# Kernel optimization log

Hardware: AMD Instinct MI355X
Metric: run time of the kernel (lower is better)

## Reference

```python
import jax, jax.numpy as jnp
import numpy as np

HIDDEN = 4096
N_HEADS = 32
N_KV_HEADS = 8
HEAD_DIM = HIDDEN // N_HEADS  # 128
ROPE_THETA = 10000.0
B, S = 2, 2048


def apply_rope_neox(x, positions, theta=ROPE_THETA):
    # x: [B, S, H, D], positions: [S]
    d = x.shape[-1]
    inv_freq = 1.0 / (theta ** (jnp.arange(0, d, 2, dtype=jnp.float32) / d))  # [D/2]
    freqs = positions.astype(jnp.float32)[:, None] * inv_freq                # [S, D/2]
    cos = jnp.cos(freqs)[None, :, None, :]                                   # [1,S,1,D/2]
    sin = jnp.sin(freqs)[None, :, None, :]
    x1, x2 = x[..., : d // 2], x[..., d // 2 :]
    return jnp.concatenate([x1 * cos - x2 * sin, x2 * cos + x1 * sin], axis=-1).astype(x.dtype)


def setup_inputs() -> dict:
    key = jax.random.key(0)
    k1, k2, k3 = jax.random.split(key, 3)
    positions = jnp.arange(S, dtype=jnp.int64) if jax.config.jax_enable_x64 else jnp.arange(S, dtype=jnp.int32)
    hidden_states = jax.random.normal(k1, (B, S, HIDDEN), dtype=jnp.float32)
    q_size = N_HEADS * HEAD_DIM
    kv_size = N_KV_HEADS * HEAD_DIM
    w_qkv = jax.random.normal(k2, (HIDDEN, q_size + 2 * kv_size), dtype=jnp.float32) * (HIDDEN ** -0.5)
    w_o = jax.random.normal(k3, (q_size, HIDDEN), dtype=jnp.float32) * (q_size ** -0.5)
    return {"positions": positions, "hidden_states": hidden_states, "w_qkv": w_qkv, "w_o": w_o}


def reference(positions, hidden_states, w_qkv, w_o):
    q_size = N_HEADS * HEAD_DIM
    kv_size = N_KV_HEADS * HEAD_DIM
    scaling = HEAD_DIM ** -0.5

    # Fused QKV projection
    qkv = jnp.einsum('bsh,hm->bsm', hidden_states, w_qkv)
    q = qkv[..., :q_size].reshape(B, S, N_HEADS, HEAD_DIM)
    k = qkv[..., q_size : q_size + kv_size].reshape(B, S, N_KV_HEADS, HEAD_DIM)
    v = qkv[..., q_size + kv_size :].reshape(B, S, N_KV_HEADS, HEAD_DIM)

    # Neox-style RoPE on q, k
    q = apply_rope_neox(q, positions)
    k = apply_rope_neox(k, positions)

    # GQA: repeat kv heads to match query heads
    rep = N_HEADS // N_KV_HEADS
    k = jnp.repeat(k, rep, axis=2)  # [B,S,Hq,D]
    v = jnp.repeat(v, rep, axis=2)

    # Causal attention (prefill path of PagedAttention)
    scores = jnp.einsum('bqhd,bkhd->bhqk', q, k) * scaling  # [B,H,S,S]
    causal = jnp.tril(jnp.ones((S, S), dtype=bool))
    scores = jnp.where(causal[None, None], scores, jnp.finfo(scores.dtype).min)
    probs = jax.nn.softmax(scores, axis=-1)
    attn = jnp.einsum('bhqk,bkhd->bqhd', probs, v).reshape(B, S, q_size)

    # Output projection
    out = jnp.einsum('bsm,mh->bsh', attn, w_o)
    return out
```

## Files before the change

kernel.cpp:

```cpp
#include <hip/hip_runtime.h>

#define S_LEN 2048
#define NB 2
#define NH 32
#define NKV 8
#define HD 128
#define HID 4096
#define NQKV 6144

using bf16x8 = __attribute__((ext_vector_type(8))) __bf16;
using f32x4  = __attribute__((ext_vector_type(4))) float;

__device__ __forceinline__ ushort f2b(float f) {
  uint u = __builtin_bit_cast(uint, f);
  u += 0x7fffu + ((u >> 16) & 1u);
  return (ushort)(u >> 16);
}
__device__ __forceinline__ float b2f(ushort h) {
  uint u = ((uint)h) << 16;
  return __builtin_bit_cast(float, u);
}

__device__ __forceinline__ uint cvt_pk_bf16(float lo, float hi) {
  uint r;
  asm("v_cvt_pk_bf16_f32 %0, %1, %2" : "=v"(r) : "v"(lo), "v"(hi));
  return r;
}

__device__ __forceinline__ void gld16(const void* g, void* l) {
  __builtin_amdgcn_global_load_lds((const __attribute__((address_space(1))) void*)g,
                                   (__attribute__((address_space(3))) void*)l, 16, 0, 0);
}

__device__ __forceinline__ void stc(float* C, size_t i, float v)  { C[i] = v; }
__device__ __forceinline__ void stc(ushort* C, size_t i, float v) { C[i] = f2b(v); }

__global__ void cvt_bf16(const float* __restrict__ src, ushort* __restrict__ dst, int n) {
  int i = (blockIdx.x * 256 + threadIdx.x) * 4;
  if (i < n) {
    float4 v = *(const float4*)(src + i);
    *(ushort4*)(dst + i) = make_ushort4(f2b(v.x), f2b(v.y), f2b(v.z), f2b(v.w));
  }
}

__global__ void trans_f32_bf16(const float* __restrict__ src, ushort* __restrict__ dst,
                               int R, int C) {
  __shared__ float tile[32][33];
  const int c0 = blockIdx.x * 32, r0 = blockIdx.y * 32;
  const int x = threadIdx.x, y = threadIdx.y;
#pragma unroll
  for (int i = 0; i < 32; i += 8)
    tile[y + i][x] = src[(size_t)(r0 + y + i) * C + (c0 + x)];
  __syncthreads();
#pragma unroll
  for (int i = 0; i < 32; i += 8)
    dst[(size_t)(c0 + y + i) * R + (r0 + x)] = f2b(tile[x][y + i]);
}

__device__ __forceinline__ void stage_tile(const ushort* __restrict__ A,
                                           const ushort* __restrict__ Bt,
                                           int lda, int ldb, int m0, int n0, int kt,
                                           ushort* dA, ushort* dB, int wave, int lane) {
#pragma unroll
  for (int h = 0; h < 4; ++h) {
    const int cb = h * 256 + wave * 64;
    const int c = cb + lane;
    const int row = c >> 3;
    const int kc = (c & 7) ^ (row & 7);
    gld16(A  + (size_t)(m0 + row) * lda + kt + kc * 8, dA + cb * 8);
    gld16(Bt + (size_t)(n0 + row) * ldb + kt + kc * 8, dB + cb * 8);
  }
}

template <typename OutT>
__global__ __launch_bounds__(256, 2) void gemm_p2(const ushort* __restrict__ A,
                                                  const ushort* __restrict__ Bt,
                                                  OutT* __restrict__ C,
                                                  int M, int Ncol, int K,
                                                  int lda, int ldb) {
  __shared__ ushort As[2][128 * 64];
  __shared__ ushort Bs[2][128 * 64];
  const int tid = threadIdx.x, wave = tid >> 6, lane = tid & 63;
  const int lr = lane & 15, lg = lane >> 4;
  const int wm = wave >> 1, wn = wave & 1;
  const int m0 = blockIdx.y * 128, n0 = blockIdx.x * 128;

  f32x4 acc[4][4];
#pragma unroll
  for (int i = 0; i < 4; ++i)
#pragma unroll
    for (int j = 0; j < 4; ++j) acc[i][j] = (f32x4){0.f, 0.f, 0.f, 0.f};

  const int NT = K >> 6;

  stage_tile(A, Bt, lda, ldb, m0, n0, 0, As[0], Bs[0], wave, lane);

  for (int it = 0; it < NT; ++it) {
    const int buf = it & 1;
    if (it + 1 < NT) {
      stage_tile(A, Bt, lda, ldb, m0, n0, (it + 1) << 6, As[buf ^ 1], Bs[buf ^ 1],
                 wave, lane);
      asm volatile("s_waitcnt vmcnt(8)" ::: "memory");
    } else {
      asm volatile("s_waitcnt vmcnt(0)" ::: "memory");
    }
    asm volatile("s_barrier" ::: "memory");

#pragma unroll
    for (int kk = 0; kk < 2; ++kk) {
      bf16x8 af[4], bfr[4];
#pragma unroll
      for (int f = 0; f < 4; ++f) {
        const int row = wm * 64 + f * 16 + lr;
        af[f] = *(const bf16x8*)(&As[buf][row * 64 + (((kk * 4 + lg) ^ (lr & 7)) << 3)]);
      }
#pragma unroll
      for (int g = 0; g < 4; ++g) {
        const int row = wn * 64 + g * 16 + lr;
        bfr[g] = *(const bf16x8*)(&Bs[buf][row * 64 + (((kk * 4 + lg) ^ (lr & 7)) << 3)]);
      }
      __builtin_amdgcn_s_setprio(1);
#pragma unroll
      for (int f = 0; f < 4; ++f)
#pragma unroll
        for (int g = 0; g < 4; ++g)
          acc[f][g] = __builtin_amdgcn_mfma_f32_16x16x32_bf16(af[f], bfr[g], acc[f][g], 0, 0, 0);
      __builtin_amdgcn_s_setprio(0);
    }
    asm volatile("s_barrier" ::: "memory");
  }

#pragma unroll
  for (int f = 0; f < 4; ++f)
#pragma unroll
    for (int g = 0; g < 4; ++g)
#pragma unroll
      for (int r = 0; r < 4; ++r) {
        const int row = m0 + wm * 64 + f * 16 + lg * 4 + r;
        const int col = n0 + wn * 64 + g * 16 + lr;
        stc(C, (size_t)row * Ncol + col, acc[f][g][r]);
      }
}

__global__ __launch_bounds__(256) void rope_qk(ushort* __restrict__ qkv) {
  int t = blockIdx.x * 256 + threadIdx.x;
  const int i = t & 63;
  t >>= 6;
  const int head  = t % (NH + NKV);
  const int token = t / (NH + NKV);
  const int s = token & (S_LEN - 1);
  const size_t base = (size_t)token * NQKV + (head < NH ? head * HD : HID + (head - NH) * HD);
  const float x1 = b2f(qkv[base + i]);
  const float x2 = b2f(qkv[base + 64 + i]);
  const float invf = exp2f(-(float)i * 0.2076205059304602f);
  const float fr = (float)s * invf;
  float cs, sn;
  sincosf(fr, &sn, &cs);
  float o1 = x1 * cs - x2 * sn;
  float o2 = x2 * cs + x1 * sn;
  if (head < NH) {
    o1 *= 0.08838834764831845f;
    o2 *= 0.08838834764831845f;
  }
  qkv[base + i]      = f2b(o1);
  qkv[base + 64 + i] = f2b(o2);
}

__global__ void vtrans(const ushort* __restrict__ qkv, ushort* __restrict__ Vt) {
  __shared__ ushort tile[32][33];
  const int dt = blockIdx.x * 32, st = blockIdx.y * 32, bk = blockIdx.z;
  const int b = bk >> 3, kv = bk & 7;
  const int x = threadIdx.x, y = threadIdx.y;
#pragma unroll
  for (int i = 0; i < 32; i += 8)
    tile[y + i][x] =
        qkv[(size_t)(b * S_LEN + st + y + i) * NQKV + 5120 + kv * HD + dt + x];
  __syncthreads();
#pragma unroll
  for (int i = 0; i < 32; i += 8)
    Vt[((size_t)bk * HD + dt + y + i) * S_LEN + st + x] = tile[x][y + i];
}

__global__ __launch_bounds__(256) void attn_fa(ushort* __restrict__ qkv,
                                               const ushort* __restrict__ Vt) {
  const int lin = blockIdx.x + 32 * blockIdx.y + 256 * blockIdx.z;
  const int swz = (lin & 7) * 64 + (lin >> 3);
  const int qp = swz & 31;
  const int g  = swz >> 5;
  const int kvh = g & 7;
  const int b   = g >> 3;

  const int wid  = threadIdx.x >> 6;
  const int lane = threadIdx.x & 63;
  const int lr = lane & 15, lg = lane >> 4;
  const int h  = kvh * 4 + wid;

  const ushort* K = qkv + (size_t)(b * S_LEN) * NQKV + HID + kvh * HD;
  const ushort* V = Vt + (size_t)(b * NKV + kvh) * (HD * S_LEN);

  __shared__ ushort Ks[2][32 * 128];
  __shared__ ushort Vs[2][128 * 32];
  __shared__ ushort P[4][16 * 40];

  for (int seg = 0; seg < 2; ++seg) {
    const int qt = seg ? (63 - qp) : qp;
    const int q0 = qt * 32;
    const ushort* Q = qkv + (size_t)(b * S_LEN + q0) * NQKV + h * HD;

    bf16x8 qf[2][4];
#pragma unroll
    for (int t = 0; t < 2; ++t)
#pragma unroll
      for (int kb = 0; kb < 4; ++kb)
        qf[t][kb] = *(const bf16x8*)(Q + (size_t)(t * 16 + lr) * NQKV + kb * 32 + lg * 8);

    f32x4 o[2][8];
#pragma unroll
    for (int t = 0; t < 2; ++t)
#pragma unroll
      for (int c = 0; c < 8; ++c) o[t][c] = (f32x4){0.f, 0.f, 0.f, 0.f};
    float mi[2]  = {-1e30f, -1e30f};
    float lip[2] = {0.f, 0.f};

    const int NTk = qt + 1;

#pragma unroll
    for (int it = 0; it < 2; ++it) {
      const int cb = it * 256 + wid * 64;
      const int d = cb + lane;
      const int krow = d >> 4, kslot = d & 15;
      gld16(K + (size_t)krow * NQKV + ((kslot ^ (krow & 15)) * 8), &Ks[0][cb * 8]);
      const int vrow = d >> 2, vslot = d & 3;
      gld16(V + (size_t)vrow * S_LEN + ((vslot ^ ((vrow >> 1) & 3)) * 8), &Vs[0][cb * 8]);
    }

    for (int itk = 0; itk < NTk; ++itk) {
      const int k0 = itk << 5;
      const int bufi = itk & 1;
      if (itk + 1 < NTk) {
        const int kn = k0 + 32;
#pragma unroll
        for (int it = 0; it < 2; ++it) {
          const int cb = it * 256 + wid * 64;
          const int d = cb + lane;
          const int krow = d >> 4, kslot = d & 15;
          gld16(K + (size_t)(kn + krow) * NQKV + ((kslot ^ (krow & 15)) * 8),
                &Ks[bufi ^ 1][cb * 8]);
          const int vrow = d >> 2, vslot = d & 3;
          gld16(V + (size_t)vrow * S_LEN + kn + ((vslot ^ ((vrow >> 1) & 3)) * 8),
                &Vs[bufi ^ 1][cb * 8]);
        }
        asm volatile("s_waitcnt vmcnt(4)" ::: "memory");
      } else {
        asm volatile("s_waitcnt vmcnt(0)" ::: "memory");
      }
      asm volatile("s_barrier" ::: "memory");

      bf16x8 kf[2][4];
#pragma unroll
      for (int u = 0; u < 2; ++u)
#pragma unroll
        for (int kb = 0; kb < 4; ++kb)
          kf[u][kb] = *(const bf16x8*)(
              &Ks[bufi][(u * 16 + lr) * 128 + (((kb * 4 + lg) ^ lr) << 3)]);

      f32x4 s[2][2];
#pragma unroll
      for (int t = 0; t < 2; ++t)
#pragma unroll
        for (int u = 0; u < 2; ++u) s[t][u] = (f32x4){0.f, 0.f, 0.f, 0.f};

      __builtin_amdgcn_s_setprio(1);
#pragma unroll
      for (int kb = 0; kb < 4; ++kb) {
        s[0][0] = __builtin_amdgcn_mfma_f32_16x16x32_bf16(kf[0][kb], qf[0][kb], s[0][0], 0, 0, 0);
        s[1][0] = __builtin_amdgcn_mfma_f32_16x16x32_bf16(kf[0][kb], qf[1][kb], s[1][0], 0, 0, 0);
        s[0][1] = __builtin_amdgcn_mfma_f32_16x16x32_bf16(kf[1][kb], qf[0][kb], s[0][1], 0, 0, 0);
        s[1][1] = __builtin_amdgcn_mfma_f32_16x16x32_bf16(kf[1][kb], qf[1][kb], s[1][1], 0, 0, 0);
      }
      __builtin_amdgcn_s_setprio(0);

      if (k0 == q0) {
#pragma unroll
        for (int t = 0; t < 2; ++t)
#pragma unroll
          for (int u = 0; u < 2; ++u)
#pragma unroll
            for (int r = 0; r < 4; ++r)
              if (u * 16 + lg * 4 + r > t * 16 + lr) s[t][u][r] = -1e30f;
      }

      float pm[2];
#pragma unroll
      for (int t = 0; t < 2; ++t) {
        float a = fmaxf(fmaxf(s[t][0][0], s[t][0][1]), fmaxf(s[t][0][2], s[t][0][3]));
        float c = fmaxf(fmaxf(s[t][1][0], s[t][1][1]), fmaxf(s[t][1][2], s[t][1][3]));
        pm[t] = fmaxf(a, c);
      }

      if (__any((pm[0] > mi[0] + 8.f) || (pm[1] > mi[1] + 8.f))) {
#pragma unroll
        for (int t = 0; t < 2; ++t) {
          float m = pm[t];
          m = fmaxf(m, __shfl_xor(m, 16));
          m = fmaxf(m, __shfl_xor(m, 32));
          const float mn = fmaxf(mi[t], m);
          const float al = __expf(mi[t] - mn);
          mi[t] = mn;
          lip[t] *= al;
#pragma unroll
          for (int r = 0; r < 4; ++r) {
            const float ar = __shfl(al, lg * 4 + r);
#pragma unroll
            for (int c = 0; c < 8; ++c) o[t][c][r] *= ar;
          }
        }
      }

#pragma unroll
      for (int t = 0; t < 2; ++t) {
        float p[2][4];
#pragma unroll
        for (int u = 0; u < 2; ++u)
#pragma unroll
          for (int r = 0; r < 4; ++r) p[u][r] = __expf(s[t][u][r] - mi[t]);
        lip[t] += ((p[0][0] + p[0][1]) + (p[0][2] + p[0][3])) +
                  ((p[1][0] + p[1][1]) + (p[1][2] + p[1][3]));
#pragma unroll
        for (int u = 0; u < 2; ++u) {
          const uint w0 = cvt_pk_bf16(p[u][0], p[u][1]);
          const uint w1 = cvt_pk_bf16(p[u][2], p[u][3]);
          *(uint2*)(&P[wid][0] + lr * 40 + u * 16 + lg * 4) = make_uint2(w0, w1);
        }
        const bf16x8 pa = *(const bf16x8*)(&P[wid][0] + lr * 40 + lg * 8);

        __builtin_amdgcn_s_setprio(1);
#pragma unroll
        for (int c = 0; c < 8; ++c) {
          const bf16x8 vf = *(const bf16x8*)(
              &Vs[bufi][(c * 16 + lr) * 32 + ((lg ^ ((lr >> 1) & 3)) << 3)]);
          o[t][c] = __builtin_amdgcn_mfma_f32_16x16x32_bf16(pa, vf, o[t][c], 0, 0, 0);
        }
        __builtin_amdgcn_s_setprio(0);
      }

      asm volatile("s_barrier" ::: "memory");
    }

    float linv[2];
#pragma unroll
    for (int t = 0; t < 2; ++t) {
      float rt = lip[t];
      rt += __shfl_xor(rt, 16);
      rt += __shfl_xor(rt, 32);
      linv[t] = 1.f / rt;
    }
#pragma unroll
    for (int t = 0; t < 2; ++t) {
#pragma unroll
      for (int r = 0; r < 4; ++r) {
        const float ir = __shfl(linv[t], lg * 4 + r);
        const size_t row = (size_t)(b * S_LEN + q0 + t * 16 + lg * 4 + r) * NQKV + h * HD;
#pragma unroll
        for (int c = 0; c < 8; ++c) qkv[row + c * 16 + lr] = f2b(o[t][c][r] * ir);
      }
    }
  }
}

extern "C" void kernel_launch(void* const* d_in, const int* in_sizes, int n_in,
                              void* d_out, int out_size, void* d_ws, size_t ws_size,
                              hipStream_t stream) {
  const float* hidden = (const float*)d_in[1];
  const float* w_qkv  = (const float*)d_in[2];
  const float* w_o    = (const float*)d_in[3];
  float* out = (float*)d_out;
  char* ws = (char*)d_ws;

  ushort* wqkvT = (ushort*)(ws);
  ushort* Vt    = (ushort*)(ws);
  ushort* hb    = (ushort*)(ws + (48u << 20));
  ushort* woT   = (ushort*)(ws + (48u << 20));
  ushort* qkvb  = (ushort*)(ws + (80u << 20));

  trans_f32_bf16<<<dim3(192, 128), dim3(32, 8), 0, stream>>>(w_qkv, wqkvT, HID, NQKV);
  cvt_bf16<<<16384, 256, 0, stream>>>(hidden, hb, NB * S_LEN * HID);
  gemm_p2<ushort><<<dim3(48, 32), 256, 0, stream>>>(
      hb, wqkvT, qkvb, NB * S_LEN, NQKV, HID, HID, HID);
  rope_qk<<<40960, 256, 0, stream>>>(qkvb);
  vtrans<<<dim3(4, 64, 16), dim3(32, 8), 0, stream>>>(qkvb, Vt);
  trans_f32_bf16<<<dim3(128, 128), dim3(32, 8), 0, stream>>>(w_o, woT, HID, HID);
  attn_fa<<<dim3(32, 8, 2), 256, 0, stream>>>(qkvb, Vt);
  gemm_p2<float><<<dim3(32, 32), 256, 0, stream>>>(
      qkvb, woT, out, NB * S_LEN, HID, HID, NQKV, HID);
}
```

Baseline: 789.4 us.

## Widen GEMM tiles to 128x256 with K=32 stages and 1x4 wave layout

Replaces the 128x128x64 GEMM tile with a 128x256x32 tile. Each wave now covers all 128 rows and a 64-column strip, doubling its accumulator count to 32 MFMA tiles. The goal is more MFMA work per LDS fragment load and fewer blocks. In exchange, twice as many barrier-separated iterations run with less work each, register pressure is higher, and the QKV and output GEMMs get fewer blocks (768 and 512), which may underfill the CUs.

```diff
diff --git a/kernel.cpp b/kernel.cpp
--- a/kernel.cpp
+++ b/kernel.cpp
@@ -57,86 +57,85 @@
     dst[(size_t)(c0 + y + i) * R + (r0 + x)] = f2b(tile[x][y + i]);
 }
 
-__device__ __forceinline__ void stage_tile(const ushort* __restrict__ A,
-                                           const ushort* __restrict__ Bt,
-                                           int lda, int ldb, int m0, int n0, int kt,
-                                           ushort* dA, ushort* dB, int wave, int lane) {
-#pragma unroll
-  for (int h = 0; h < 4; ++h) {
-    const int cb = h * 256 + wave * 64;
-    const int c = cb + lane;
-    const int row = c >> 3;
-    const int kc = (c & 7) ^ (row & 7);
-    gld16(A  + (size_t)(m0 + row) * lda + kt + kc * 8, dA + cb * 8);
-    gld16(Bt + (size_t)(n0 + row) * ldb + kt + kc * 8, dB + cb * 8);
-  }
-}
-
 template <typename OutT>
-__global__ __launch_bounds__(256, 2) void gemm_p2(const ushort* __restrict__ A,
+__global__ __launch_bounds__(256, 2) void gemm_p3(const ushort* __restrict__ A,
                                                   const ushort* __restrict__ Bt,
                                                   OutT* __restrict__ C,
                                                   int M, int Ncol, int K,
                                                   int lda, int ldb) {
-  __shared__ ushort As[2][128 * 64];
-  __shared__ ushort Bs[2][128 * 64];
+  __shared__ ushort As[2][128 * 32];
+  __shared__ ushort Bs[2][256 * 32];
   const int tid = threadIdx.x, wave = tid >> 6, lane = tid & 63;
   const int lr = lane & 15, lg = lane >> 4;
-  const int wm = wave >> 1, wn = wave & 1;
-  const int m0 = blockIdx.y * 128, n0 = blockIdx.x * 128;
-
-  f32x4 acc[4][4];
-#pragma unroll
-  for (int i = 0; i < 4; ++i)
+  const int wn = wave;
+  const int m0 = blockIdx.y * 128, n0 = blockIdx.x * 256;
+
+  f32x4 acc[8][4];
+#pragma unroll
+  for (int i = 0; i < 8; ++i)
 #pragma unroll
     for (int j = 0; j < 4; ++j) acc[i][j] = (f32x4){0.f, 0.f, 0.f, 0.f};
 
-  const int NT = K >> 6;
-
-  stage_tile(A, Bt, lda, ldb, m0, n0, 0, As[0], Bs[0], wave, lane);
+  const int NT = K >> 5;
+
+  auto stage = [&](int kt, int bufi) {
+#pragma unroll
+    for (int it = 0; it < 2; ++it) {
+      const int cb = it * 256 + wave * 64;
+      const int c = cb + lane;
+      const int row = c >> 2, kc = (c & 3) ^ (row & 3);
+      gld16(A + (size_t)(m0 + row) * lda + kt + kc * 8, &As[bufi][cb * 8]);
+    }
+#pragma unroll
+    for (int it = 0; it < 4; ++it) {
+      const int cb = it * 256 + wave * 64;
+      const int c = cb + lane;
+      const int row = c >> 2, kc = (c & 3) ^ (row & 3);
+      gld16(Bt + (size_t)(n0 + row) * ldb + kt + kc * 8, &Bs[bufi][cb * 8]);
+    }
+  };
+
+  stage(0, 0);
 
   for (int it = 0; it < NT; ++it) {
     const int buf = it & 1;
     if (it + 1 < NT) {
-      stage_tile(A, Bt, lda, ldb, m0, n0, (it + 1) << 6, As[buf ^ 1], Bs[buf ^ 1],
-                 wave, lane);
-      asm volatile("s_waitcnt vmcnt(8)" ::: "memory");
+      stage((it + 1) << 5, buf ^ 1);
+      asm volatile("s_waitcnt vmcnt(6)" ::: "memory");
     } else {
       asm volatile("s_waitcnt vmcnt(0)" ::: "memory");
     }
     asm volatile("s_barrier" ::: "memory");
 
-#pragma unroll
-    for (int kk = 0; kk < 2; ++kk) {
-      bf16x8 af[4], bfr[4];
-#pragma unroll
-      for (int f = 0; f < 4; ++f) {
-        const int row = wm * 64 + f * 16 + lr;
-        af[f] = *(const bf16x8*)(&As[buf][row * 64 + (((kk * 4 + lg) ^ (lr & 7)) << 3)]);
-      }
-#pragma unroll
-      for (int g = 0; g < 4; ++g) {
-        const int row = wn * 64 + g * 16 + lr;
-        bfr[g] = *(const bf16x8*)(&Bs[buf][row * 64 + (((kk * 4 + lg) ^ (lr & 7)) << 3)]);
-      }
-      __builtin_amdgcn_s_setprio(1);
-#pragma unroll
-      for (int f = 0; f < 4; ++f)
-#pragma unroll
-        for (int g = 0; g < 4; ++g)
-          acc[f][g] = __builtin_amdgcn_mfma_f32_16x16x32_bf16(af[f], bfr[g], acc[f][g], 0, 0, 0);
-      __builtin_amdgcn_s_setprio(0);
-    }
+    bf16x8 af[8], bfr[4];
+#pragma unroll
+    for (int f = 0; f < 8; ++f) {
+      const int row = f * 16 + lr;
+      af[f] = *(const bf16x8*)(&As[buf][row * 32 + ((lg ^ (lr & 3)) << 3)]);
+    }
+#pragma unroll
+    for (int g = 0; g < 4; ++g) {
+      const int row = wn * 64 + g * 16 + lr;
+      bfr[g] = *(const bf16x8*)(&Bs[buf][row * 32 + ((lg ^ (lr & 3)) << 3)]);
+    }
+    __builtin_amdgcn_s_setprio(1);
+#pragma unroll
+    for (int f = 0; f < 8; ++f)
+#pragma unroll
+      for (int g = 0; g < 4; ++g)
+        acc[f][g] = __builtin_amdgcn_mfma_f32_16x16x32_bf16(af[f], bfr[g], acc[f][g], 0, 0, 0);
+    __builtin_amdgcn_s_setprio(0);
+
     asm volatile("s_barrier" ::: "memory");
   }
 
 #pragma unroll
-  for (int f = 0; f < 4; ++f)
+  for (int f = 0; f < 8; ++f)
 #pragma unroll
     for (int g = 0; g < 4; ++g)
 #pragma unroll
       for (int r = 0; r < 4; ++r) {
-        const int row = m0 + wm * 64 + f * 16 + lg * 4 + r;
+        const int row = m0 + f * 16 + lg * 4 + r;
         const int col = n0 + wn * 64 + g * 16 + lr;
         stc(C, (size_t)row * Ncol + col, acc[f][g][r]);
       }
@@ -385,12 +384,12 @@
 
   trans_f32_bf16<<<dim3(192, 128), dim3(32, 8), 0, stream>>>(w_qkv, wqkvT, HID, NQKV);
   cvt_bf16<<<16384, 256, 0, stream>>>(hidden, hb, NB * S_LEN * HID);
-  gemm_p2<ushort><<<dim3(48, 32), 256, 0, stream>>>(
+  gemm_p3<ushort><<<dim3(24, 32), 256, 0, stream>>>(
       hb, wqkvT, qkvb, NB * S_LEN, NQKV, HID, HID, HID);
   rope_qk<<<40960, 256, 0, stream>>>(qkvb);
   vtrans<<<dim3(4, 64, 16), dim3(32, 8), 0, stream>>>(qkvb, Vt);
   trans_f32_bf16<<<dim3(128, 128), dim3(32, 8), 0, stream>>>(w_o, woT, HID, HID);
   attn_fa<<<dim3(32, 8, 2), 256, 0, stream>>>(qkvb, Vt);
-  gemm_p2<float><<<dim3(32, 32), 256, 0, stream>>>(
+  gemm_p3<float><<<dim3(16, 32), 256, 0, stream>>>(
       qkvb, woT, out, NB * S_LEN, HID, HID, NQKV, HID);
 }
```

Result: slower. 843.7 us (+6.9%).
